# Performance work log

Hardware: AMD Instinct MI355X
Metric: run time of the kernel (lower is better)

The kernel has to match this reference:

```python
import jax, jax.numpy as jnp
import numpy as np


def setup_inputs() -> dict:
    key = jax.random.key(0)
    kx, ky = jax.random.split(key)
    n, m, d = 2048, 2048, 16  # d == n_wires
    x = jax.random.normal(kx, (n, d), dtype=jnp.float32)
    y = jax.random.normal(ky, (m, d), dtype=jnp.float32)
    return {"x": x, "y": y}


def reference(x, y):
    # RY gates on distinct wires commute; RY(-y_k) RY(x_k) = RY(x_k - y_k).
    # State = tensor product over wires of RY(x_k - y_k)|0>, so the |0...0>
    # amplitude is prod_k cos((x_k - y_k)/2). Original code stores abs(amplitude).
    half_diff = 0.5 * (x[:, None, :] - y[None, :, :])  # [n, m, d]
    kernel = jnp.abs(jnp.prod(jnp.cos(half_diff), axis=-1))  # [n, m]
    return kernel
```

## Files before the change

### kernel.cpp

```cpp
#include <hip/hip_runtime.h>
#include <hip/hip_bf16.h>


constexpr int D = 16;
constexpr int RSTR = 72;

typedef short  bf16x8 __attribute__((ext_vector_type(8)));
typedef float  f32x16 __attribute__((ext_vector_type(16)));

static __device__ inline unsigned int pk2(float a, float b) {
    __hip_bfloat16 ha = __float2bfloat16(a);
    __hip_bfloat16 hb = __float2bfloat16(b);
    unsigned short ua, ub;
    __builtin_memcpy(&ua, &ha, 2);
    __builtin_memcpy(&ub, &hb, 2);
    return (unsigned int)ua | ((unsigned int)ub << 16);
}

__global__ __launch_bounds__(256)
void qkern(const float* __restrict__ x, const float* __restrict__ y,
           float* __restrict__ out, int m) {
    __shared__ unsigned short Al[64 * RSTR];
    __shared__ unsigned short Bl[64 * RSTR];

    const int tid   = threadIdx.x;
    const int row0b = blockIdx.x * 64;
    const int col0b = blockIdx.y * 64;

    {
        const int u    = tid >> 1;
        const int half = tid & 1;
        const bool isrow = (u < 64);
        const float* src = isrow ? (x + (size_t)(row0b + u) * D)
                                 : (y + (size_t)(col0b + (u - 64)) * D);
        unsigned short* dst = (isrow ? Al + (size_t)u * RSTR
                                     : Bl + (size_t)(u - 64) * RSTR);
        const float scale = isrow ? 0.5f : 1.0f;

        float f[4][4];
#pragma unroll
        for (int pp = 0; pp < 4; ++pp) {
            const int p = half * 4 + pp;
            const float a0 = src[2 * p], a1 = src[2 * p + 1];
            float sm, cm, sp, cp;
            __sincosf(0.5f * (a0 - a1), &sm, &cm);
            __sincosf(0.5f * (a0 + a1), &sp, &cp);
            f[pp][0] = scale * cm; f[pp][1] = scale * sm;
            f[pp][2] = scale * cp; f[pp][3] = scale * sp;
        }
#pragma unroll
        for (int qq = 0; qq < 2; ++qq) {
            const int q = half * 2 + qq;
            const float* fa = f[2 * qq];
            const float* fb = f[2 * qq + 1];
            uint4 lo, hi;
            lo.x = pk2(fa[0] * fb[0], fa[0] * fb[1]);
            lo.y = pk2(fa[0] * fb[2], fa[0] * fb[3]);
            lo.z = pk2(fa[1] * fb[0], fa[1] * fb[1]);
            lo.w = pk2(fa[1] * fb[2], fa[1] * fb[3]);
            hi.x = pk2(fa[2] * fb[0], fa[2] * fb[1]);
            hi.y = pk2(fa[2] * fb[2], fa[2] * fb[3]);
            hi.z = pk2(fa[3] * fb[0], fa[3] * fb[1]);
            hi.w = pk2(fa[3] * fb[2], fa[3] * fb[3]);
            *(uint4*)(dst + q * 16)     = lo;
            *(uint4*)(dst + q * 16 + 8) = hi;
        }
    }
    __syncthreads();

    const int wave = tid >> 6;
    const int lane = tid & 63;
    const int l31  = lane & 31;
    const int kh   = lane >> 5;
    const int rw   = (wave >> 1) * 32;
    const int cw   = (wave & 1) * 32;

    const f32x16 zc = {0.f};

    f32x16 prod;
    {
        const bf16x8 a0 = *(const bf16x8*)(Al + (size_t)(rw + l31) * RSTR + 0 * 16 + kh * 8);
        const bf16x8 b0 = *(const bf16x8*)(Bl + (size_t)(cw + l31) * RSTR + 0 * 16 + kh * 8);
        prod = __builtin_amdgcn_mfma_f32_32x32x16_bf16(a0, b0, zc, 0, 0, 0);
    }
#pragma unroll
    for (int q = 1; q < 4; ++q) {
        const bf16x8 aq = *(const bf16x8*)(Al + (size_t)(rw + l31) * RSTR + q * 16 + kh * 8);
        const bf16x8 bq = *(const bf16x8*)(Bl + (size_t)(cw + l31) * RSTR + q * 16 + kh * 8);
        const f32x16 acc = __builtin_amdgcn_mfma_f32_32x32x16_bf16(aq, bq, zc, 0, 0, 0);
        prod *= acc;
    }

    const int ocol = col0b + cw + l31;
    float* base = out + (size_t)(row0b + rw + 4 * kh) * m + ocol;
#pragma unroll
    for (int r = 0; r < 16; ++r) {
        const int row_off = (r & 3) + 8 * (r >> 2);
        __builtin_nontemporal_store(fabsf(prod[r]), base + (size_t)row_off * m);
    }
}

extern "C" void kernel_launch(void* const* d_in, const int* in_sizes, int n_in,
                              void* d_out, int out_size, void* d_ws, size_t ws_size,
                              hipStream_t stream) {
    const float* x = (const float*)d_in[0];
    const float* y = (const float*)d_in[1];
    float* out = (float*)d_out;
    const int n = in_sizes[0] / D;
    const int m = in_sizes[1] / D;

    dim3 grid(n / 64, m / 64);
    qkern<<<grid, 256, 0, stream>>>(x, y, out, m);
}
```

Before: 60.95 us.

## Precompute factor tables in a separate kernel and read them from global memory

The per-vector sincos and bf16 pair-product factors move into a prepass kernel that writes them once to global tables laid out in MFMA operand order. Before, every tile block recomputed these factors for its 64 rows and 64 columns, which duplicated the trig work across the whole grid. The main kernel now loads operands straight from global memory with no LDS staging and no barrier, and runs its four MFMAs independently. The cost is a second kernel launch, a round trip of the tables through global memory, and fixed-size device tables sized for 2048 vectors.

```diff
diff --git a/kernel.cpp b/kernel.cpp
--- a/kernel.cpp
+++ b/kernel.cpp
@@ -3,10 +3,12 @@
 
 
 constexpr int D = 16;
-constexpr int RSTR = 72;
 
 typedef short  bf16x8 __attribute__((ext_vector_type(8)));
 typedef float  f32x16 __attribute__((ext_vector_type(16)));
+
+__device__ __align__(16) unsigned short Atab[64 * 2048];
+__device__ __align__(16) unsigned short Btab[64 * 2048];
 
 static __device__ inline unsigned int pk2(float a, float b) {
     __hip_bfloat16 ha = __float2bfloat16(a);
@@ -18,81 +20,81 @@
 }
 
 __global__ __launch_bounds__(256)
-void qkern(const float* __restrict__ x, const float* __restrict__ y,
-           float* __restrict__ out, int m) {
-    __shared__ unsigned short Al[64 * RSTR];
-    __shared__ unsigned short Bl[64 * RSTR];
+void qfact(const float* __restrict__ x, const float* __restrict__ y, int n) {
+    const int tid  = blockIdx.x * 256 + threadIdx.x;
+    const int u    = tid >> 1;
+    const int half = tid & 1;
+    const bool isrow = (u < n);
+    const int  v   = isrow ? u : u - n;
+    const float* src = (isrow ? x : y) + (size_t)v * D;
+    unsigned short* tab = isrow ? Atab : Btab;
+    const float scale = isrow ? 0.5f : 1.0f;
 
-    const int tid   = threadIdx.x;
-    const int row0b = blockIdx.x * 64;
-    const int col0b = blockIdx.y * 64;
+    float e[8];
+    *(float4*)(e)     = *(const float4*)(src + 8 * half);
+    *(float4*)(e + 4) = *(const float4*)(src + 8 * half + 4);
 
-    {
-        const int u    = tid >> 1;
-        const int half = tid & 1;
-        const bool isrow = (u < 64);
-        const float* src = isrow ? (x + (size_t)(row0b + u) * D)
-                                 : (y + (size_t)(col0b + (u - 64)) * D);
-        unsigned short* dst = (isrow ? Al + (size_t)u * RSTR
-                                     : Bl + (size_t)(u - 64) * RSTR);
-        const float scale = isrow ? 0.5f : 1.0f;
+    float f[4][4];
+#pragma unroll
+    for (int pp = 0; pp < 4; ++pp) {
+        const float a0 = e[2 * pp], a1 = e[2 * pp + 1];
+        float sm, cm, sp, cp;
+        __sincosf(0.5f * (a0 - a1), &sm, &cm);
+        __sincosf(0.5f * (a0 + a1), &sp, &cp);
+        f[pp][0] = scale * cm; f[pp][1] = scale * sm;
+        f[pp][2] = scale * cp; f[pp][3] = scale * sp;
+    }
 
-        float f[4][4];
+    unsigned short* dst = tab + (size_t)(v >> 5) * 2048 + (size_t)(v & 31) * 8;
 #pragma unroll
-        for (int pp = 0; pp < 4; ++pp) {
-            const int p = half * 4 + pp;
-            const float a0 = src[2 * p], a1 = src[2 * p + 1];
-            float sm, cm, sp, cp;
-            __sincosf(0.5f * (a0 - a1), &sm, &cm);
-            __sincosf(0.5f * (a0 + a1), &sp, &cp);
-            f[pp][0] = scale * cm; f[pp][1] = scale * sm;
-            f[pp][2] = scale * cp; f[pp][3] = scale * sp;
-        }
-#pragma unroll
-        for (int qq = 0; qq < 2; ++qq) {
-            const int q = half * 2 + qq;
-            const float* fa = f[2 * qq];
-            const float* fb = f[2 * qq + 1];
-            uint4 lo, hi;
-            lo.x = pk2(fa[0] * fb[0], fa[0] * fb[1]);
-            lo.y = pk2(fa[0] * fb[2], fa[0] * fb[3]);
-            lo.z = pk2(fa[1] * fb[0], fa[1] * fb[1]);
-            lo.w = pk2(fa[1] * fb[2], fa[1] * fb[3]);
-            hi.x = pk2(fa[2] * fb[0], fa[2] * fb[1]);
-            hi.y = pk2(fa[2] * fb[2], fa[2] * fb[3]);
-            hi.z = pk2(fa[3] * fb[0], fa[3] * fb[1]);
-            hi.w = pk2(fa[3] * fb[2], fa[3] * fb[3]);
-            *(uint4*)(dst + q * 16)     = lo;
-            *(uint4*)(dst + q * 16 + 8) = hi;
-        }
+    for (int qq = 0; qq < 2; ++qq) {
+        const int q = half * 2 + qq;
+        const float* fa = f[2 * qq];
+        const float* fb = f[2 * qq + 1];
+        uint4 lo, hi;
+        lo.x = pk2(fa[0] * fb[0], fa[0] * fb[1]);
+        lo.y = pk2(fa[0] * fb[2], fa[0] * fb[3]);
+        lo.z = pk2(fa[1] * fb[0], fa[1] * fb[1]);
+        lo.w = pk2(fa[1] * fb[2], fa[1] * fb[3]);
+        hi.x = pk2(fa[2] * fb[0], fa[2] * fb[1]);
+        hi.y = pk2(fa[2] * fb[2], fa[2] * fb[3]);
+        hi.z = pk2(fa[3] * fb[0], fa[3] * fb[1]);
+        hi.w = pk2(fa[3] * fb[2], fa[3] * fb[3]);
+        *(uint4*)(dst + (size_t)(q * 2 + 0) * 256) = lo;
+        *(uint4*)(dst + (size_t)(q * 2 + 1) * 256) = hi;
     }
-    __syncthreads();
+}
 
-    const int wave = tid >> 6;
-    const int lane = tid & 63;
+__global__ __launch_bounds__(256)
+void qmain(float* __restrict__ out, int m) {
+    const int wave = threadIdx.x >> 6;
+    const int lane = threadIdx.x & 63;
     const int l31  = lane & 31;
     const int kh   = lane >> 5;
-    const int rw   = (wave >> 1) * 32;
-    const int cw   = (wave & 1) * 32;
+    const int rb   = blockIdx.x * 2 + (wave >> 1);
+    const int cb   = blockIdx.y * 2 + (wave & 1);
+
+    const unsigned short* abase = Atab + (size_t)rb * 2048 + (size_t)kh * 256 + (size_t)l31 * 8;
+    const unsigned short* bbase = Btab + (size_t)cb * 2048 + (size_t)kh * 256 + (size_t)l31 * 8;
+
+    bf16x8 a0 = *(const bf16x8*)(abase);
+    bf16x8 b0 = *(const bf16x8*)(bbase);
+    bf16x8 a1 = *(const bf16x8*)(abase + 512);
+    bf16x8 b1 = *(const bf16x8*)(bbase + 512);
+    bf16x8 a2 = *(const bf16x8*)(abase + 1024);
+    bf16x8 b2 = *(const bf16x8*)(bbase + 1024);
+    bf16x8 a3 = *(const bf16x8*)(abase + 1536);
+    bf16x8 b3 = *(const bf16x8*)(bbase + 1536);
 
     const f32x16 zc = {0.f};
+    f32x16 q0 = __builtin_amdgcn_mfma_f32_32x32x16_bf16(a0, b0, zc, 0, 0, 0);
+    f32x16 q1 = __builtin_amdgcn_mfma_f32_32x32x16_bf16(a1, b1, zc, 0, 0, 0);
+    f32x16 q2 = __builtin_amdgcn_mfma_f32_32x32x16_bf16(a2, b2, zc, 0, 0, 0);
+    f32x16 q3 = __builtin_amdgcn_mfma_f32_32x32x16_bf16(a3, b3, zc, 0, 0, 0);
+    const f32x16 prod = (q0 * q1) * (q2 * q3);
 
-    f32x16 prod;
-    {
-        const bf16x8 a0 = *(const bf16x8*)(Al + (size_t)(rw + l31) * RSTR + 0 * 16 + kh * 8);
-        const bf16x8 b0 = *(const bf16x8*)(Bl + (size_t)(cw + l31) * RSTR + 0 * 16 + kh * 8);
-        prod = __builtin_amdgcn_mfma_f32_32x32x16_bf16(a0, b0, zc, 0, 0, 0);
-    }
-#pragma unroll
-    for (int q = 1; q < 4; ++q) {
-        const bf16x8 aq = *(const bf16x8*)(Al + (size_t)(rw + l31) * RSTR + q * 16 + kh * 8);
-        const bf16x8 bq = *(const bf16x8*)(Bl + (size_t)(cw + l31) * RSTR + q * 16 + kh * 8);
-        const f32x16 acc = __builtin_amdgcn_mfma_f32_32x32x16_bf16(aq, bq, zc, 0, 0, 0);
-        prod *= acc;
-    }
-
-    const int ocol = col0b + cw + l31;
-    float* base = out + (size_t)(row0b + rw + 4 * kh) * m + ocol;
+    const int ocol = cb * 32 + l31;
+    float* base = out + (size_t)(rb * 32 + 4 * kh) * m + ocol;
 #pragma unroll
     for (int r = 0; r < 16; ++r) {
         const int row_off = (r & 3) + 8 * (r >> 2);
@@ -109,6 +111,9 @@
     const int n = in_sizes[0] / D;
     const int m = in_sizes[1] / D;
 
+    const int nvec = n + m;
+    qfact<<<dim3((nvec * 2) / 256), 256, 0, stream>>>(x, y, n);
+
     dim3 grid(n / 64, m / 64);
-    qkern<<<grid, 256, 0, stream>>>(x, y, out, m);
+    qmain<<<grid, 256, 0, stream>>>(out, m);
 }
```

After: 62.50 us. +2.5%, slower.
